# Kernel tuning notes

Hardware: AMD Instinct MI355X
Metric: run time of the kernel (lower is better)

The kernel has to match this reference:

```python
import jax, jax.numpy as jnp
import numpy as np


def setup_inputs() -> dict:
    key = jax.random.key(0)
    k0, k1, k2, k3, k4, k5 = jax.random.split(key, 6)
    N, E, F, D, H = 50000, 1000000, 128, 32, 4
    # xavier_normal with gain = calculate_gain('relu') = sqrt(2)
    std = np.sqrt(2.0) * np.sqrt(2.0 / (F + D))
    return {
        "entity_features": jax.random.normal(k0, (N, 1, F), jnp.float32),
        "relation_features": jax.random.normal(k1, (E, 1, F), jnp.float32),
        "src": jax.random.randint(k2, (E,), 0, N, jnp.int32),
        "dst": jax.random.randint(k3, (E,), 0, N, jnp.int32),
        "w_q": jax.random.normal(k4, (H, F, D), jnp.float32) * std,
        "w_k": jax.random.normal(k5, (H, F, D), jnp.float32) * std,
    }


def reference(entity_features, relation_features, src, dst, w_q, w_k):
    # entity_features: (N, 1, F) -> repeat over heads is just a broadcast
    feat = entity_features[:, 0, :]        # (N, F)
    rel = relation_features[:, 0, :]       # (E, F)
    num_heads = w_q.shape[0]
    N = feat.shape[0]

    # per-head projections: q = feat @ w_q, k = feat @ w_k, erel = rel @ w_k
    q = jnp.einsum("nf,hfd->nhd", feat, w_q)      # (N, H, D)  'out_el'
    k = jnp.einsum("nf,hfd->nhd", feat, w_k)      # (N, H, D)  'out_er'
    erel = jnp.einsum("ef,hfd->ehd", rel, w_k)    # (E, H, D)  'out_erel'

    # v_dot_u: dst's out_er . src's out_el ; e_dot_u: edge out_erel . src's out_er
    e = (jnp.einsum("ehd,ehd->eh", k[dst], q[src])
         + jnp.einsum("ehd,ehd->eh", erel, k[src]))   # (E, H)
    e = jax.nn.leaky_relu(e, negative_slope=0.01)

    # edge_softmax normalized by source node (softmax over outgoing edges)
    m = jax.ops.segment_max(e, src, num_segments=N)   # (N, H)
    m = jnp.where(jnp.isfinite(m), m, jnp.zeros_like(m))
    ex = jnp.exp(e - m[src])                          # (E, H)
    denom = jax.ops.segment_sum(ex, src, num_segments=N)  # (N, H)
    att = ex / denom[src]                             # (E, H)

    # squeeze(-1).sum(-1)/num_heads on the (E, H, 1) edge tensor -> mean over heads
    return att.sum(axis=-1) / num_heads               # (E,)
```

## Files before the change

### kernel.cpp

```cpp
#include <hip/hip_runtime.h>

#define HH 4
#define FF 128
#define DD 32

typedef float f32x4 __attribute__((ext_vector_type(4)));


__global__ void zero_kernel(int* __restrict__ c, int n) {
    int i = blockIdx.x * blockDim.x + threadIdx.x;
    if (i < n) c[i] = 0;
}

__global__ __launch_bounds__(256) void scan_partial_kernel(int* __restrict__ partial, int nb) {
    __shared__ int sm[256];
    int t = threadIdx.x;
    int v = (t < nb) ? partial[t] : 0;
    sm[t] = v; __syncthreads();
    for (int off = 1; off < 256; off <<= 1) {
        int x = (t >= off) ? sm[t - off] : 0;
        __syncthreads();
        sm[t] += x;
        __syncthreads();
    }
    if (t < nb) partial[t] = sm[t] - v;
}

__global__ void addback_kernel(int* __restrict__ start, int* __restrict__ cursor,
                               const int* __restrict__ partial, int N) {
    int gid = blockIdx.x * 256 + threadIdx.x;
    if (gid < N) {
        int s = start[gid] + partial[blockIdx.x];
        start[gid] = s;
        cursor[gid] = s;
    }
}

__global__ void scatter_kernel(const int* __restrict__ src, const int* __restrict__ dst,
                               int* __restrict__ cursor, int* __restrict__ perm,
                               int* __restrict__ dsts, int E) {
    int i = blockIdx.x * blockDim.x + threadIdx.x;
    if (i >= E) return;
    int s = src[i];
    int pos = atomicAdd(&cursor[s], 1);
    perm[pos] = i;
    dsts[pos] = dst[i];
}


__global__ __launch_bounds__(256) void qk_hist_kernel(
    const float* __restrict__ feat, const float* __restrict__ wq,
    const float* __restrict__ wk, float* __restrict__ q,
    float* __restrict__ k, int N,
    const int* __restrict__ src, int* __restrict__ counts, int E, int QKB) {
    __shared__ float fs[32 * FF];
    int bid = blockIdx.x;
    if (bid >= QKB) {
        int i = ((bid - QKB) * 256 + threadIdx.x) * 4;
        if (i + 3 < E) {
            int4 v = *(const int4*)(src + i);
            atomicAdd(&counts[v.x], 1);
            atomicAdd(&counts[v.y], 1);
            atomicAdd(&counts[v.z], 1);
            atomicAdd(&counts[v.w], 1);
        } else {
            for (; i < E; ++i) atomicAdd(&counts[src[i]], 1);
        }
        return;
    }
    int n0 = bid * 32;
    int nb = N - n0; if (nb > 32) nb = 32;
    const float4* s4 = (const float4*)(feat + (size_t)n0 * FF);
    int nf4 = nb * FF / 4;
    for (int i = threadIdx.x; i < nf4; i += 256) ((float4*)fs)[i] = s4[i];
    __syncthreads();

    int isK = threadIdx.x >> 7;
    int o   = threadIdx.x & 127;
    int h = o >> 5, d = o & 31;
    const float* w = (isK ? wk : wq) + ((size_t)h * FF) * DD + d;

    float acc[32];
#pragma unroll
    for (int e = 0; e < 32; ++e) acc[e] = 0.f;
    for (int f = 0; f < FF; f += 4) {
        float w0 = w[(f + 0) * DD], w1 = w[(f + 1) * DD];
        float w2 = w[(f + 2) * DD], w3 = w[(f + 3) * DD];
#pragma unroll
        for (int e = 0; e < 32; ++e) {
            float4 fv = *(const float4*)&fs[e * FF + f];
            acc[e] += fv.x * w0 + fv.y * w1 + fv.z * w2 + fv.w * w3;
        }
    }
    float* outp = isK ? k : q;
    for (int e = 0; e < nb; ++e)
        outp[((size_t)(n0 + e) * HH + h) * DD + d] = acc[e];
}


__global__ __launch_bounds__(256) void kk_scan_kernel(
    const float* __restrict__ kbuf, const float* __restrict__ wk,
    float* __restrict__ kkout, int N,
    const int* __restrict__ counts, int* __restrict__ startb,
    int* __restrict__ partial, int KKB) {
    __shared__ float ks[16 * FF];
    __shared__ int sm[256];
    int bid = blockIdx.x;
    if (bid >= KKB) {
        int b = bid - KKB;
        int tid = threadIdx.x;
        int gid = b * 256 + tid;
        int v = gid < N ? counts[gid] : 0;
        sm[tid] = v; __syncthreads();
        for (int off = 1; off < 256; off <<= 1) {
            int x = (tid >= off) ? sm[tid - off] : 0;
            __syncthreads();
            sm[tid] += x;
            __syncthreads();
        }
        if (gid < N) startb[gid] = sm[tid] - v;
        if (tid == 255) partial[b] = sm[tid];
        return;
    }
    int n0 = bid * 16;
    int nb = N - n0; if (nb > 16) nb = 16;
    const float4* s4 = (const float4*)(kbuf + (size_t)n0 * FF);
    int nf4 = nb * FF / 4;
    for (int i = threadIdx.x; i < nf4; i += 256) ((float4*)ks)[i] = s4[i];
    __syncthreads();

    int o = threadIdx.x;
    int h1 = o >> 7, f1 = o & 127;
    int h2 = h1 + 2;
    const float* w1 = wk + ((size_t)h1 * FF + f1) * DD;
    const float* w2 = wk + ((size_t)h2 * FF + f1) * DD;

    float acc1[16], acc2[16];
#pragma unroll
    for (int e = 0; e < 16; ++e) { acc1[e] = 0.f; acc2[e] = 0.f; }
    for (int d = 0; d < DD; d += 4) {
        float4 wv1 = *(const float4*)&w1[d];
        float4 wv2 = *(const float4*)&w2[d];
#pragma unroll
        for (int e = 0; e < 16; ++e) {
            float4 k1 = *(const float4*)&ks[e * FF + h1 * DD + d];
            float4 k2 = *(const float4*)&ks[e * FF + h2 * DD + d];
            acc1[e] += k1.x * wv1.x + k1.y * wv1.y + k1.z * wv1.z + k1.w * wv1.w;
            acc2[e] += k2.x * wv2.x + k2.y * wv2.y + k2.z * wv2.z + k2.w * wv2.w;
        }
    }
    for (int e = 0; e < nb; ++e) {
        kkout[((size_t)(n0 + e) * HH + h1) * FF + f1] = acc1[e];
        kkout[((size_t)(n0 + e) * HH + h2) * FF + f1] = acc2[e];
    }
}


__device__ __forceinline__ int score4(
    const float* __restrict__ rel, const float* __restrict__ k,
    int pv, int dv, int j0, int g, int t,
    const float4* kkA, const float4* kkB, const float2* qv,
    float* ev, int* e_i_out) {
    int idx = j0 + g;
    int e_i = __shfl(pv, idx, 64);
    int dd  = __shfl(dv, idx, 64);
    *e_i_out = e_i;
    const float* rp = rel + (size_t)e_i * FF + t * 8;
    f32x4 r0 = __builtin_nontemporal_load((const f32x4*)rp);
    f32x4 r1 = __builtin_nontemporal_load((const f32x4*)(rp + 4));
#pragma unroll
    for (int h = 0; h < HH; ++h) {
        float2 kv = *(const float2*)(k + ((size_t)dd * HH + h) * DD + t * 2);
        float a = r0.x * kkA[h].x + r0.y * kkA[h].y + r0.z * kkA[h].z + r0.w * kkA[h].w
                + r1.x * kkB[h].x + r1.y * kkB[h].y + r1.z * kkB[h].z + r1.w * kkB[h].w
                + qv[h].x * kv.x + qv[h].y * kv.y;
#pragma unroll
        for (int off = 1; off < 16; off <<= 1) a += __shfl_xor(a, off, 64);
        ev[h] = a >= 0.f ? a : 0.01f * a;
    }
    return idx;
}

__global__ __launch_bounds__(256) void group_kernel(
    const float* __restrict__ rel, const int* __restrict__ perm,
    const int* __restrict__ dsts, const float* __restrict__ q,
    const float* __restrict__ k, const float* __restrict__ kk,
    const int* __restrict__ start, const int* __restrict__ counts,
    float* __restrict__ out, int N) {
    __shared__ __align__(16) float e_buf_all[4][128][4];
    int wid = threadIdx.x >> 6;
    int s = blockIdx.x * 4 + wid;
    if (s >= N) return;
    int cnt = counts[s];
    if (cnt == 0) return;
    int base = start[s];
    int lane = threadIdx.x & 63;
    int g = lane >> 4, t = lane & 15;
    float (*e_buf)[4] = e_buf_all[wid];

    float4 kkA[HH], kkB[HH];
    float2 qv[HH];
    const float* kkbase = kk + (size_t)s * (HH * FF) + t * 8;
    const float* qbase  = q  + (size_t)s * (HH * DD) + t * 2;
#pragma unroll
    for (int h = 0; h < HH; ++h) {
        kkA[h] = *(const float4*)(kkbase + h * FF);
        kkB[h] = *(const float4*)(kkbase + h * FF + 4);
        qv[h]  = *(const float2*)(qbase + h * DD);
    }

    float m[HH] = {-INFINITY, -INFINITY, -INFINITY, -INFINITY};
    bool fast = (cnt <= 128);

    for (int c0 = 0; c0 < cnt; c0 += 64) {
        int nc = min(cnt - c0, 64);
        int pv = 0, dv = 0;
        if (lane < nc) { pv = perm[base + c0 + lane]; dv = dsts[base + c0 + lane]; }
        for (int j0 = 0; j0 < nc; j0 += 4) {
            float ev[HH]; int e_i;
            int idx = score4(rel, k, pv, dv, j0, g, t, kkA, kkB, qv, ev, &e_i);
            if (idx < nc) {
#pragma unroll
                for (int h = 0; h < HH; ++h) m[h] = fmaxf(m[h], ev[h]);
                if (fast && t == 0)
                    *(float4*)e_buf[c0 + idx] = make_float4(ev[0], ev[1], ev[2], ev[3]);
            }
        }
    }
#pragma unroll
    for (int h = 0; h < HH; ++h) {
        m[h] = fmaxf(m[h], __shfl_xor(m[h], 16, 64));
        m[h] = fmaxf(m[h], __shfl_xor(m[h], 32, 64));
    }

    if (fast) {
        int i0 = lane, i1 = lane + 64;
        float ex0[HH] = {0.f, 0.f, 0.f, 0.f}, ex1[HH] = {0.f, 0.f, 0.f, 0.f};
        if (i0 < cnt) {
            float4 ev = *(const float4*)e_buf[i0];
            ex0[0] = __expf(ev.x - m[0]); ex0[1] = __expf(ev.y - m[1]);
            ex0[2] = __expf(ev.z - m[2]); ex0[3] = __expf(ev.w - m[3]);
        }
        if (i1 < cnt) {
            float4 ev = *(const float4*)e_buf[i1];
            ex1[0] = __expf(ev.x - m[0]); ex1[1] = __expf(ev.y - m[1]);
            ex1[2] = __expf(ev.z - m[2]); ex1[3] = __expf(ev.w - m[3]);
        }
        float rl[HH];
#pragma unroll
        for (int h = 0; h < HH; ++h) {
            float v = ex0[h] + ex1[h];
#pragma unroll
            for (int off = 1; off < 64; off <<= 1) v += __shfl_xor(v, off, 64);
            rl[h] = 1.0f / v;
        }
        if (i0 < cnt)
            out[perm[base + i0]] = 0.25f * (ex0[0]*rl[0] + ex0[1]*rl[1] + ex0[2]*rl[2] + ex0[3]*rl[3]);
        if (i1 < cnt)
            out[perm[base + i1]] = 0.25f * (ex1[0]*rl[0] + ex1[1]*rl[1] + ex1[2]*rl[2] + ex1[3]*rl[3]);
    } else {
        float lacc[HH] = {0.f, 0.f, 0.f, 0.f};
        for (int c0 = 0; c0 < cnt; c0 += 64) {
            int nc = min(cnt - c0, 64);
            int pv = 0, dv = 0;
            if (lane < nc) { pv = perm[base + c0 + lane]; dv = dsts[base + c0 + lane]; }
            for (int j0 = 0; j0 < nc; j0 += 4) {
                float ev[HH]; int e_i;
                int idx = score4(rel, k, pv, dv, j0, g, t, kkA, kkB, qv, ev, &e_i);
                if (idx < nc && t == 0) {
#pragma unroll
                    for (int h = 0; h < HH; ++h) lacc[h] += __expf(ev[h] - m[h]);
                }
            }
        }
        float rl[HH];
#pragma unroll
        for (int h = 0; h < HH; ++h) {
            float v = lacc[h];
#pragma unroll
            for (int off = 1; off < 64; off <<= 1) v += __shfl_xor(v, off, 64);
            rl[h] = 1.0f / v;
        }
        for (int c0 = 0; c0 < cnt; c0 += 64) {
            int nc = min(cnt - c0, 64);
            int pv = 0, dv = 0;
            if (lane < nc) { pv = perm[base + c0 + lane]; dv = dsts[base + c0 + lane]; }
            for (int j0 = 0; j0 < nc; j0 += 4) {
                float ev[HH]; int e_i;
                int idx = score4(rel, k, pv, dv, j0, g, t, kkA, kkB, qv, ev, &e_i);
                if (idx < nc && t == 0) {
                    float a = __expf(ev[0]-m[0])*rl[0] + __expf(ev[1]-m[1])*rl[1]
                            + __expf(ev[2]-m[2])*rl[2] + __expf(ev[3]-m[3])*rl[3];
                    out[e_i] = 0.25f * a;
                }
            }
        }
    }
}

extern "C" void kernel_launch(void* const* d_in, const int* in_sizes, int n_in,
                              void* d_out, int out_size, void* d_ws, size_t ws_size,
                              hipStream_t stream) {
    const float* feat = (const float*)d_in[0];
    const float* rel  = (const float*)d_in[1];
    const int*   src  = (const int*)d_in[2];
    const int*   dst  = (const int*)d_in[3];
    const float* wq   = (const float*)d_in[4];
    const float* wk   = (const float*)d_in[5];
    float* out = (float*)d_out;

    const int N = in_sizes[0] / FF;
    const int E = in_sizes[2];

    float* q      = (float*)d_ws;
    float* k      = q  + (size_t)N * HH * DD;
    float* kk     = k  + (size_t)N * HH * DD;
    int*   counts = (int*)(kk + (size_t)N * HH * FF);
    int*   start  = counts + N;
    int*   cursor = start + N;
    int*   partial= cursor + N;
    int*   perm   = partial + 256;
    int*   dsts   = perm + E;

    int nb  = (N + 255) / 256;
    int QKB = (N + 31) / 32;
    int HB  = (E + 1023) / 1024;
    int KKB = (N + 15) / 16;

    zero_kernel<<<nb, 256, 0, stream>>>(counts, N);
    qk_hist_kernel<<<QKB + HB, 256, 0, stream>>>(feat, wq, wk, q, k, N, src, counts, E, QKB);
    kk_scan_kernel<<<KKB + nb, 256, 0, stream>>>(k, wk, kk, N, counts, start, partial, KKB);
    scan_partial_kernel<<<1, 256, 0, stream>>>(partial, nb);
    addback_kernel<<<nb, 256, 0, stream>>>(start, cursor, partial, N);
    scatter_kernel<<<(E + 255) / 256, 256, 0, stream>>>(src, dst, cursor, perm, dsts, E);
    group_kernel<<<(N + 3) / 4, 256, 0, stream>>>(rel, perm, dsts, q, k, kk, start, counts, out, N);
}
```

Before: 416.3 us.

## Replace global prefix scan with per-wave atomic bucket allocation and pack edge data

Replaces the three-kernel exclusive scan (block scan, partial scan, addback) with a single wave-level scan plus an atomicAdd on a global cursor that hands out contiguous bucket ranges. Segments no longer follow node order, but each node still gets a contiguous range. Perm and dst are packed into one int2 written with a nontemporal store, so the group kernel needs one 8-byte load instead of two. The group kernel now runs one 64-thread block per node, and the zero kernel becomes a memset. Two launches are removed; the cost is more atomic contention on the global cursor and many more small blocks.

```diff
diff --git a/kernel.cpp b/kernel.cpp
--- a/kernel.cpp
+++ b/kernel.cpp
@@ -7,44 +7,14 @@
 typedef float f32x4 __attribute__((ext_vector_type(4)));
 
 
-__global__ void zero_kernel(int* __restrict__ c, int n) {
-    int i = blockIdx.x * blockDim.x + threadIdx.x;
-    if (i < n) c[i] = 0;
-}
-
-__global__ __launch_bounds__(256) void scan_partial_kernel(int* __restrict__ partial, int nb) {
-    __shared__ int sm[256];
-    int t = threadIdx.x;
-    int v = (t < nb) ? partial[t] : 0;
-    sm[t] = v; __syncthreads();
-    for (int off = 1; off < 256; off <<= 1) {
-        int x = (t >= off) ? sm[t - off] : 0;
-        __syncthreads();
-        sm[t] += x;
-        __syncthreads();
-    }
-    if (t < nb) partial[t] = sm[t] - v;
-}
-
-__global__ void addback_kernel(int* __restrict__ start, int* __restrict__ cursor,
-                               const int* __restrict__ partial, int N) {
-    int gid = blockIdx.x * 256 + threadIdx.x;
-    if (gid < N) {
-        int s = start[gid] + partial[blockIdx.x];
-        start[gid] = s;
-        cursor[gid] = s;
-    }
-}
-
 __global__ void scatter_kernel(const int* __restrict__ src, const int* __restrict__ dst,
-                               int* __restrict__ cursor, int* __restrict__ perm,
-                               int* __restrict__ dsts, int E) {
+                               int* __restrict__ cursor, int2* __restrict__ ed, int E) {
     int i = blockIdx.x * blockDim.x + threadIdx.x;
     if (i >= E) return;
     int s = src[i];
     int pos = atomicAdd(&cursor[s], 1);
-    perm[pos] = i;
-    dsts[pos] = dst[i];
+    long long pack = (unsigned)i | ((long long)dst[i] << 32);
+    __builtin_nontemporal_store(pack, (long long*)&ed[pos]);
 }
 
 
@@ -98,28 +68,32 @@
 }
 
 
-__global__ __launch_bounds__(256) void kk_scan_kernel(
+__global__ __launch_bounds__(256) void kk_alloc_kernel(
     const float* __restrict__ kbuf, const float* __restrict__ wk,
     float* __restrict__ kkout, int N,
     const int* __restrict__ counts, int* __restrict__ startb,
-    int* __restrict__ partial, int KKB) {
+    int* __restrict__ cursor, int* __restrict__ gcur, int KKB) {
     __shared__ float ks[16 * FF];
-    __shared__ int sm[256];
     int bid = blockIdx.x;
     if (bid >= KKB) {
-        int b = bid - KKB;
-        int tid = threadIdx.x;
-        int gid = b * 256 + tid;
-        int v = gid < N ? counts[gid] : 0;
-        sm[tid] = v; __syncthreads();
-        for (int off = 1; off < 256; off <<= 1) {
-            int x = (tid >= off) ? sm[tid - off] : 0;
-            __syncthreads();
-            sm[tid] += x;
-            __syncthreads();
-        }
-        if (gid < N) startb[gid] = sm[tid] - v;
-        if (tid == 255) partial[b] = sm[tid];
+        int sid = (bid - KKB) * 256 + threadIdx.x;
+        int lane = threadIdx.x & 63;
+        int cnt = (sid < N) ? counts[sid] : 0;
+        int incl = cnt;
+#pragma unroll
+        for (int off = 1; off < 64; off <<= 1) {
+            int y = __shfl_up(incl, off, 64);
+            if (lane >= off) incl += y;
+        }
+        int total = __shfl(incl, 63, 64);
+        int base = 0;
+        if (lane == 63) base = atomicAdd(gcur, total);
+        base = __shfl(base, 63, 64);
+        if (sid < N) {
+            int st = base + incl - cnt;
+            startb[sid] = st;
+            cursor[sid] = st;
+        }
         return;
     }
     int n0 = bid * 16;
@@ -181,22 +155,19 @@
     return idx;
 }
 
-__global__ __launch_bounds__(256) void group_kernel(
-    const float* __restrict__ rel, const int* __restrict__ perm,
-    const int* __restrict__ dsts, const float* __restrict__ q,
-    const float* __restrict__ k, const float* __restrict__ kk,
-    const int* __restrict__ start, const int* __restrict__ counts,
-    float* __restrict__ out, int N) {
-    __shared__ __align__(16) float e_buf_all[4][128][4];
-    int wid = threadIdx.x >> 6;
-    int s = blockIdx.x * 4 + wid;
+__global__ __launch_bounds__(64) void group_kernel(
+    const float* __restrict__ rel, const int2* __restrict__ ed,
+    const float* __restrict__ q, const float* __restrict__ k,
+    const float* __restrict__ kk, const int* __restrict__ start,
+    const int* __restrict__ counts, float* __restrict__ out, int N) {
+    __shared__ __align__(16) float e_buf[128][4];
+    int s = blockIdx.x;
     if (s >= N) return;
     int cnt = counts[s];
     if (cnt == 0) return;
     int base = start[s];
-    int lane = threadIdx.x & 63;
+    int lane = threadIdx.x;
     int g = lane >> 4, t = lane & 15;
-    float (*e_buf)[4] = e_buf_all[wid];
 
     float4 kkA[HH], kkB[HH];
     float2 qv[HH];
@@ -215,7 +186,7 @@
     for (int c0 = 0; c0 < cnt; c0 += 64) {
         int nc = min(cnt - c0, 64);
         int pv = 0, dv = 0;
-        if (lane < nc) { pv = perm[base + c0 + lane]; dv = dsts[base + c0 + lane]; }
+        if (lane < nc) { int2 pd = ed[base + c0 + lane]; pv = pd.x; dv = pd.y; }
         for (int j0 = 0; j0 < nc; j0 += 4) {
             float ev[HH]; int e_i;
             int idx = score4(rel, k, pv, dv, j0, g, t, kkA, kkB, qv, ev, &e_i);
@@ -255,15 +226,15 @@
             rl[h] = 1.0f / v;
         }
         if (i0 < cnt)
-            out[perm[base + i0]] = 0.25f * (ex0[0]*rl[0] + ex0[1]*rl[1] + ex0[2]*rl[2] + ex0[3]*rl[3]);
+            out[ed[base + i0].x] = 0.25f * (ex0[0]*rl[0] + ex0[1]*rl[1] + ex0[2]*rl[2] + ex0[3]*rl[3]);
         if (i1 < cnt)
-            out[perm[base + i1]] = 0.25f * (ex1[0]*rl[0] + ex1[1]*rl[1] + ex1[2]*rl[2] + ex1[3]*rl[3]);
+            out[ed[base + i1].x] = 0.25f * (ex1[0]*rl[0] + ex1[1]*rl[1] + ex1[2]*rl[2] + ex1[3]*rl[3]);
     } else {
         float lacc[HH] = {0.f, 0.f, 0.f, 0.f};
         for (int c0 = 0; c0 < cnt; c0 += 64) {
             int nc = min(cnt - c0, 64);
             int pv = 0, dv = 0;
-            if (lane < nc) { pv = perm[base + c0 + lane]; dv = dsts[base + c0 + lane]; }
+            if (lane < nc) { int2 pd = ed[base + c0 + lane]; pv = pd.x; dv = pd.y; }
             for (int j0 = 0; j0 < nc; j0 += 4) {
                 float ev[HH]; int e_i;
                 int idx = score4(rel, k, pv, dv, j0, g, t, kkA, kkB, qv, ev, &e_i);
@@ -284,7 +255,7 @@
         for (int c0 = 0; c0 < cnt; c0 += 64) {
             int nc = min(cnt - c0, 64);
             int pv = 0, dv = 0;
-            if (lane < nc) { pv = perm[base + c0 + lane]; dv = dsts[base + c0 + lane]; }
+            if (lane < nc) { int2 pd = ed[base + c0 + lane]; pv = pd.x; dv = pd.y; }
             for (int j0 = 0; j0 < nc; j0 += 4) {
                 float ev[HH]; int e_i;
                 int idx = score4(rel, k, pv, dv, j0, g, t, kkA, kkB, qv, ev, &e_i);
@@ -316,22 +287,19 @@
     float* k      = q  + (size_t)N * HH * DD;
     float* kk     = k  + (size_t)N * HH * DD;
     int*   counts = (int*)(kk + (size_t)N * HH * FF);
-    int*   start  = counts + N;
+    int*   gcur   = counts + N;
+    int*   start  = gcur + 1;
     int*   cursor = start + N;
-    int*   partial= cursor + N;
-    int*   perm   = partial + 256;
-    int*   dsts   = perm + E;
+    int2*  ed     = (int2*)(cursor + N);
 
     int nb  = (N + 255) / 256;
     int QKB = (N + 31) / 32;
     int HB  = (E + 1023) / 1024;
     int KKB = (N + 15) / 16;
 
-    zero_kernel<<<nb, 256, 0, stream>>>(counts, N);
+    hipMemsetAsync(counts, 0, (size_t)(N + 1) * sizeof(int), stream);
     qk_hist_kernel<<<QKB + HB, 256, 0, stream>>>(feat, wq, wk, q, k, N, src, counts, E, QKB);
-    kk_scan_kernel<<<KKB + nb, 256, 0, stream>>>(k, wk, kk, N, counts, start, partial, KKB);
-    scan_partial_kernel<<<1, 256, 0, stream>>>(partial, nb);
-    addback_kernel<<<nb, 256, 0, stream>>>(start, cursor, partial, N);
-    scatter_kernel<<<(E + 255) / 256, 256, 0, stream>>>(src, dst, cursor, perm, dsts, E);
-    group_kernel<<<(N + 3) / 4, 256, 0, stream>>>(rel, perm, dsts, q, k, kk, start, counts, out, N);
-}
+    kk_alloc_kernel<<<KKB + nb, 256, 0, stream>>>(k, wk, kk, N, counts, start, cursor, gcur, KKB);
+    scatter_kernel<<<(E + 255) / 256, 256, 0, stream>>>(src, dst, cursor, ed, E);
+    group_kernel<<<N, 64, 0, stream>>>(rel, ed, q, k, kk, start, counts, out, N);
+}
```

Result: no change. 424.4 us (+2.0%).
